# Kernel optimization log

Hardware: AMD Instinct MI355X
Metric: run time of the kernel (lower is better)

Reference implementation:

```python
import jax, jax.numpy as jnp
import numpy as np

B, N, D = 2, 2048, 1024
H, ENC = 16, 8
HD = D // H
EPS = 1e-5


def _apply_rope(x, cos, sin):
    # x: [B,N,H,HD], cos/sin: [N,HD//2]
    c = cos[None, :, None, :]
    s = sin[None, :, None, :]
    x_re = x[..., 0::2]
    x_im = x[..., 1::2]
    out = jnp.stack([x_re * c - x_im * s, x_re * s + x_im * c], axis=-1)
    return out.reshape(x.shape)


def _rmsnorm(x):
    return x * jax.lax.rsqrt(jnp.mean(x * x, axis=-1, keepdims=True) + EPS)


def setup_inputs() -> dict:
    key = jax.random.key(0)
    ks = jax.random.split(key, 8)
    pos = jnp.arange(N, dtype=jnp.float32)[:, None]
    inv_freq = 1.0 / (10000.0 ** (jnp.arange(0, HD, 2, dtype=jnp.float32) / HD))  # [HD//2]
    ang = pos * inv_freq[None, :]
    std = 0.02
    return {
        "x": jax.random.normal(ks[0], (B, N, D), dtype=jnp.float32),
        "rope_cos": jnp.cos(ang),
        "rope_sin": jnp.sin(ang),
        "Wq": std * jax.random.normal(ks[1], (D, D), dtype=jnp.float32),
        "Wk": std * jax.random.normal(ks[2], (D, D), dtype=jnp.float32),
        "Wv": std * jax.random.normal(ks[3], (D, D), dtype=jnp.float32),
        "Wo_enc": std * jax.random.normal(ks[4], (H * HD, D), dtype=jnp.float32),
        "Wo_dec": std * jax.random.normal(ks[5], ((H - ENC) * HD, D), dtype=jnp.float32),
        "heads": H,
        "encoder_heads": ENC,
    }


def reference(x, rope_cos, rope_sin, Wq, Wk, Wv, Wo_enc, Wo_dec, heads, encoder_heads):
    b, n, d = x.shape
    hd = d // heads
    scale = hd ** (-0.5)
    q = (x @ Wq).reshape(b, n, heads, hd)
    k = (x @ Wk).reshape(b, n, heads, hd)
    v = (x @ Wv).reshape(b, n, heads, hd)
    q = _rmsnorm(_apply_rope(q, rope_cos, rope_sin))
    k = _rmsnorm(_apply_rope(k, rope_cos, rope_sin))
    # scores: [B,H,N,N]
    scores = jnp.einsum("bihd,bjhd->bhij", q, k) * scale
    causal = jnp.tril(jnp.ones((n, n), dtype=bool))  # [N,N]
    is_enc = (jnp.arange(heads) < encoder_heads)[:, None, None]  # [H,1,1]
    allow = jnp.logical_or(is_enc, causal[None, :, :])  # [H,N,N]
    scores = jnp.where(allow[None], scores, -jnp.inf)
    att = jax.nn.softmax(scores, axis=-1)
    out = jnp.einsum("bhij,bjhd->bihd", att, v)  # [B,N,H,HD]
    enc_out = out.reshape(b, n, heads * hd) @ Wo_enc
    dec_out = out[:, :, encoder_heads:, :].reshape(b, n, (heads - encoder_heads) * hd) @ Wo_dec
    return (enc_out, dec_out)
```

## Files before the change

kernel.cpp:

```cpp
#include <hip/hip_runtime.h>
#include <hip/hip_bf16.h>
#include <math.h>

#define B_    2
#define N_    2048
#define D_    1024
#define H_    16
#define ENC_  8
#define HD_   64
#define EPS_  1e-5f
#define M_    (B_ * N_)

typedef __bf16 bf16x8 __attribute__((ext_vector_type(8)));
typedef __bf16 bf16x2 __attribute__((ext_vector_type(2)));
typedef float  f32x4  __attribute__((ext_vector_type(4)));

#define MB(x) ((size_t)(x) * 1024 * 1024)

#define KSC_  0.18033688011112042f

__device__ __forceinline__ void gld16(const __bf16* g, __bf16* l) {
    __builtin_amdgcn_global_load_lds(
        (const __attribute__((address_space(1))) void*)g,
        (__attribute__((address_space(3))) void*)l,
        16, 0, 0);
}

template <typename OutT>
__device__ __forceinline__ void gemm_core(
    const __bf16* __restrict__ A, const __bf16* __restrict__ Bt,
    OutT* __restrict__ C, int K, int lda, int aoff, int ldc,
    int bm, int bn, __bf16* As, __bf16* Bs)
{
    const int tid  = threadIdx.x;
    const int w    = tid >> 6;
    const int lane = tid & 63;
    const int lrow = lane & 15;
    const int quad = lane >> 4;
    const int wr   = w >> 1;
    const int wc   = w & 1;

    const int sr = lane >> 2;
    const int sc = (lane & 3) * 8;
    const __bf16* Ag0 = A  + (size_t)(bm +      w * 16 + sr) * lda + aoff + sc;
    const __bf16* Ag1 = A  + (size_t)(bm + 64 + w * 16 + sr) * lda + aoff + sc;
    const __bf16* Bg0 = Bt + (size_t)(bn +      w * 16 + sr) * K + sc;
    const __bf16* Bg1 = Bt + (size_t)(bn + 64 + w * 16 + sr) * K + sc;
    __bf16* Al0 = &As[w * 512];
    __bf16* Al1 = &As[2048 + w * 512];
    __bf16* Bl0 = &Bs[w * 512];
    __bf16* Bl1 = &Bs[2048 + w * 512];

    f32x4 acc[4][4];
    #pragma unroll
    for (int i = 0; i < 4; ++i)
        #pragma unroll
        for (int j = 0; j < 4; ++j) acc[i][j] = (f32x4){0.f, 0.f, 0.f, 0.f};

    for (int k0 = 0; k0 < K; k0 += 32) {
        gld16(Ag0 + k0, Al0);
        gld16(Ag1 + k0, Al1);
        gld16(Bg0 + k0, Bl0);
        gld16(Bg1 + k0, Bl1);
        __syncthreads();

        bf16x8 af[4], bf[4];
        #pragma unroll
        for (int rt = 0; rt < 4; ++rt)
            af[rt] = *(const bf16x8*)&As[(wr * 64 + rt * 16 + lrow) * 32 + quad * 8];
        #pragma unroll
        for (int ct = 0; ct < 4; ++ct)
            bf[ct] = *(const bf16x8*)&Bs[(wc * 64 + ct * 16 + lrow) * 32 + quad * 8];

        #pragma unroll
        for (int rt = 0; rt < 4; ++rt)
            #pragma unroll
            for (int ct = 0; ct < 4; ++ct)
                acc[rt][ct] = __builtin_amdgcn_mfma_f32_16x16x32_bf16(
                    af[rt], bf[ct], acc[rt][ct], 0, 0, 0);
        __syncthreads();
    }

    #pragma unroll
    for (int rt = 0; rt < 4; ++rt)
        #pragma unroll
        for (int ct = 0; ct < 4; ++ct)
            #pragma unroll
            for (int r = 0; r < 4; ++r) {
                const int row = bm + wr * 64 + rt * 16 + quad * 4 + r;
                const int col = bn + wc * 64 + ct * 16 + lrow;
                C[(size_t)row * ldc + col] = (OutT)acc[rt][ct][r];
            }
}

__global__ __launch_bounds__(256) void gemm_qkv(
    const __bf16* __restrict__ A, const __bf16* __restrict__ Bt,
    __bf16* __restrict__ C)
{
    __shared__ __bf16 As[128 * 32];
    __shared__ __bf16 Bs[128 * 32];
    gemm_core<__bf16>(A, Bt, C, D_, D_, 0, 3072,
                      blockIdx.y * 128, blockIdx.x * 128, As, Bs);
}

__global__ __launch_bounds__(256) void gemm_out(
    const __bf16* __restrict__ A, const __bf16* __restrict__ Woe,
    const __bf16* __restrict__ Wod, float* __restrict__ Cenc,
    float* __restrict__ Cdec)
{
    __shared__ __bf16 As[128 * 32];
    __shared__ __bf16 Bs[128 * 32];
    const int bx = blockIdx.x;
    if (bx < 8) {
        gemm_core<float>(A, Woe, Cenc, 1024, D_, 0, D_,
                         blockIdx.y * 128, bx * 128, As, Bs);
    } else {
        gemm_core<float>(A, Wod, Cdec, 512, D_, 512, D_,
                         blockIdx.y * 128, (bx - 8) * 128, As, Bs);
    }
}

__global__ __launch_bounds__(256) void f32_to_bf16(
    const float* __restrict__ src, __bf16* __restrict__ dst)
{
    const size_t i = ((size_t)blockIdx.x * 256 + threadIdx.x) * 8;
    float4 a = *(const float4*)&src[i];
    float4 b = *(const float4*)&src[i + 4];
    bf16x8 o = {(__bf16)a.x, (__bf16)a.y, (__bf16)a.z, (__bf16)a.w,
                (__bf16)b.x, (__bf16)b.y, (__bf16)b.z, (__bf16)b.w};
    *(bf16x8*)&dst[i] = o;
}

struct WtArgs {
    const float* W[5];
    __bf16*      Wt[5];
    int          K[5];
    int          nyb[5];
};

__global__ __launch_bounds__(256) void wt_conv_all(WtArgs a)
{
    const int z = blockIdx.z;
    if (blockIdx.y >= a.nyb[z]) return;
    const float* W  = a.W[z];
    __bf16*      Wt = a.Wt[z];
    const int    K  = a.K[z];

    __shared__ __bf16 t[64][72];
    const int kb = blockIdx.y * 64;
    const int nb = blockIdx.x * 64;
    {
        const int kl = threadIdx.x >> 2;
        const int c0 = (threadIdx.x & 3) * 16;
        const float* src = W + (size_t)(kb + kl) * D_ + nb + c0;
        #pragma unroll
        for (int u = 0; u < 4; ++u) {
            float4 f = *(const float4*)&src[u * 4];
            t[c0 + u * 4 + 0][kl] = (__bf16)f.x;
            t[c0 + u * 4 + 1][kl] = (__bf16)f.y;
            t[c0 + u * 4 + 2][kl] = (__bf16)f.z;
            t[c0 + u * 4 + 3][kl] = (__bf16)f.w;
        }
    }
    __syncthreads();
    {
        const int nl  = threadIdx.x >> 2;
        const int k0c = (threadIdx.x & 3) * 16;
        __bf16* dst = Wt + (size_t)(nb + nl) * K + kb + k0c;
        *(bf16x8*)&dst[0] = *(const bf16x8*)&t[nl][k0c];
        *(bf16x8*)&dst[8] = *(const bf16x8*)&t[nl][k0c + 8];
    }
}

__global__ __launch_bounds__(256) void rope_vconv(
    const __bf16* __restrict__ qkv,
    const float* __restrict__ cs, const float* __restrict__ sn,
    __bf16* __restrict__ qbf, __bf16* __restrict__ kbf,
    __bf16* __restrict__ vt)
{
    if (blockIdx.x < 16384) {
        const int row  = blockIdx.x * 4 + (threadIdx.x >> 6);
        const int lane = threadIdx.x & 63;
        const int n    = (row >> 4) & (N_ - 1);
        const int b    = row >> 15;
        const int h    = row & 15;
        const int p    = lane >> 1;

        const float c = cs[n * (HD_ / 2) + p];
        const float s = sn[n * (HD_ / 2) + p];
        const size_t ibase = (size_t)(b * N_ + n) * 3072 + h * HD_ + lane;
        const size_t obase = ((size_t)(b * H_ + h) * N_ + n) * HD_ + lane;
        const bool odd = (lane & 1);

        {
            float val = (float)qkv[ibase];
            float partner = __shfl_xor(val, 1, 64);
            float r = odd ? fmaf(partner, s, val * c)
                          : (val * c - partner * s);
            float ss = r * r;
            #pragma unroll
            for (int off = 1; off < 64; off <<= 1) ss += __shfl_xor(ss, off, 64);
            qbf[obase] = (__bf16)(r * rsqrtf(ss * (1.0f / 64.0f) + EPS_) * KSC_);
        }
        {
            float val = (float)qkv[ibase + 1024];
            float partner = __shfl_xor(val, 1, 64);
            float r = odd ? fmaf(partner, s, val * c)
                          : (val * c - partner * s);
            float ss = r * r;
            #pragma unroll
            for (int off = 1; off < 64; off <<= 1) ss += __shfl_xor(ss, off, 64);
            kbf[obase] = (__bf16)(r * rsqrtf(ss * (1.0f / 64.0f) + EPS_));
        }
    } else {
        __shared__ __bf16 tile[64][72];
        const int bx = blockIdx.x - 16384;
        const int bh = bx >> 5;
        const int b  = bh >> 4, h = bh & 15;
        const int n0 = (bx & 31) * 64;
        {
            const int nl = threadIdx.x >> 2;
            const int d0 = (threadIdx.x & 3) * 16;
            const __bf16* src =
                qkv + (size_t)(b * N_ + n0 + nl) * 3072 + 2048 + h * HD_ + d0;
            bf16x8 v0 = *(const bf16x8*)&src[0];
            bf16x8 v1 = *(const bf16x8*)&src[8];
            #pragma unroll
            for (int e = 0; e < 8; ++e) {
                tile[d0 + e][nl]     = v0[e];
                tile[d0 + 8 + e][nl] = v1[e];
            }
        }
        __syncthreads();
        {
            const int dl = threadIdx.x >> 2;
            const int nc = (threadIdx.x & 3) * 16;
            __bf16* dst = vt + ((size_t)(bh * HD_ + dl)) * N_ + n0 + nc;
            bf16x8 o0, o1;
            #pragma unroll
            for (int e = 0; e < 8; ++e) {
                const int p0 = nc + e;
                const int p1 = nc + 8 + e;
                o0[e] = tile[dl][(p0 & ~31) + ((p0 & 31) >> 1) + 16 * (p0 & 1)];
                o1[e] = tile[dl][(p1 & ~31) + ((p1 & 31) >> 1) + 16 * (p1 & 1)];
            }
            *(bf16x8*)&dst[0] = o0;
            *(bf16x8*)&dst[8] = o1;
        }
    }
}

__global__ __launch_bounds__(256) void attn_mfma(
    const __bf16* __restrict__ qbf, const __bf16* __restrict__ kbf,
    const __bf16* __restrict__ vtbf, __bf16* __restrict__ o)
{
    __shared__ __bf16 Ks[2][4096];
    __shared__ __bf16 Vs[2][4096];
    __shared__ __bf16 Plds[4][16][36];

    const int tid  = threadIdx.x;
    const int w    = tid >> 6;
    const int lane = tid & 63;
    const int lrow = lane & 15;
    const int quad = lane >> 4;

    int bh, nwork, qbs[2];
    if (blockIdx.x < 512) {
        const int e = blockIdx.x & 15;
        bh = (e >> 3) * 16 + (e & 7);
        qbs[0] = blockIdx.x >> 4;
        qbs[1] = 0;
        nwork = 1;
    } else {
        const int idx = blockIdx.x - 512;
        const int d = idx & 15;
        bh = (d >> 3) * 16 + 8 + (d & 7);
        const int p = idx >> 4;
        qbs[0] = 31 - p;
        qbs[1] = p;
        nwork = 2;
    }
    const int b = bh >> 4, h = bh & 15;
    const bool enc = (h < ENC_);
    const bool dec = !enc;

    const __bf16* qbase = qbf  + (size_t)bh * N_ * HD_;
    const __bf16* kbase = kbf  + (size_t)bh * N_ * HD_;
    const __bf16* vbase = vtbf + (size_t)bh * HD_ * N_;

    const __bf16* kg0 = kbase + (size_t)lane * HD_ + w * 8;
    const __bf16* kg1 = kbase + (size_t)lane * HD_ + (w + 4) * 8;
    const __bf16* vg  = vbase + (size_t)lane * N_;

    const f32x4 zero = {0.f, 0.f, 0.f, 0.f};

    for (int wi = 0; wi < nwork; ++wi) {
        const int qb = qbs[wi];
        const int i0 = qb * 64 + w * 16;
        const int ntiles = enc ? (N_ >> 6) : (qb + 1);

        bf16x8 qf[2];
        #pragma unroll
        for (int kc = 0; kc < 2; ++kc)
            qf[kc] = *(const bf16x8*)
                &qbase[(size_t)(i0 + lrow) * HD_ + kc * 32 + quad * 8];

        f32x4 oacc[4];
        #pragma unroll
        for (int c = 0; c < 4; ++c) oacc[c] = zero;
        float lsum[4] = {};

        auto stage = [&](int t, int bb) {
            const int j0 = t << 6;
            gld16(kg0 + (size_t)j0 * HD_, &Ks[bb][(w)     * 512]);
            gld16(kg1 + (size_t)j0 * HD_, &Ks[bb][(w + 4) * 512]);
            gld16(vg + j0 + w * 8,        &Vs[bb][(w)     * 512]);
            gld16(vg + j0 + (w + 4) * 8,  &Vs[bb][(w + 4) * 512]);
        };

        if (wi) __syncthreads();
        stage(0, 0);
        for (int t = 0; t < ntiles; ++t) {
            const int bb = t & 1;
            __syncthreads();
            if (t + 1 < ntiles) stage(t + 1, bb ^ 1);

            #pragma unroll
            for (int s = 0; s < 2; ++s) {
                const int jp = (t << 6) + s * 32;

                bf16x8 kf0 = *(const bf16x8*)&Ks[bb][((quad)     * 64 + s * 32 + lrow) * 8];
                bf16x8 kf1 = *(const bf16x8*)&Ks[bb][((4 + quad) * 64 + s * 32 + lrow) * 8];
                bf16x8 kf2 = *(const bf16x8*)&Ks[bb][((quad)     * 64 + s * 32 + 16 + lrow) * 8];
                bf16x8 kf3 = *(const bf16x8*)&Ks[bb][((4 + quad) * 64 + s * 32 + 16 + lrow) * 8];

                f32x4 s0 = zero, s1 = zero;
                s0 = __builtin_amdgcn_mfma_f32_16x16x32_bf16(qf[0], kf0, s0, 0, 0, 0);
                s0 = __builtin_amdgcn_mfma_f32_16x16x32_bf16(qf[1], kf1, s0, 0, 0, 0);
                s1 = __builtin_amdgcn_mfma_f32_16x16x32_bf16(qf[0], kf2, s1, 0, 0, 0);
                s1 = __builtin_amdgcn_mfma_f32_16x16x32_bf16(qf[1], kf3, s1, 0, 0, 0);

                if (dec && (jp + 31 > i0)) {
                    #pragma unroll
                    for (int r = 0; r < 4; ++r) {
                        const int i  = i0 + quad * 4 + r;
                        float pA = (jp + lrow      <= i) ? exp2f(s0[r]) : 0.f;
                        float pB = (jp + 16 + lrow <= i) ? exp2f(s1[r]) : 0.f;
                        lsum[r] += pA + pB;
                        bf16x2 pp = {(__bf16)pA, (__bf16)pB};
                        *(bf16x2*)&Plds[w][quad * 4 + r][2 * lrow] = pp;
                    }
                } else {
                    #pragma unroll
                    for (int r = 0; r < 4; ++r) {
                        float pA = exp2f(s0[r]);
                        float pB = exp2f(s1[r]);
                        lsum[r] += pA + pB;
                        bf16x2 pp = {(__bf16)pA, (__bf16)pB};
                        *(bf16x2*)&Plds[w][quad * 4 + r][2 * lrow] = pp;
                    }
                }

                bf16x8 vf0 = *(const bf16x8*)&Vs[bb][((s * 4 + quad) * 64 +  0 + lrow) * 8];
                bf16x8 vf1 = *(const bf16x8*)&Vs[bb][((s * 4 + quad) * 64 + 16 + lrow) * 8];
                bf16x8 vf2 = *(const bf16x8*)&Vs[bb][((s * 4 + quad) * 64 + 32 + lrow) * 8];
                bf16x8 vf3 = *(const bf16x8*)&Vs[bb][((s * 4 + quad) * 64 + 48 + lrow) * 8];

                bf16x8 pf = *(const bf16x8*)&Plds[w][lrow][quad * 8];
                oacc[0] = __builtin_amdgcn_mfma_f32_16x16x32_bf16(pf, vf0, oacc[0], 0, 0, 0);
                oacc[1] = __builtin_amdgcn_mfma_f32_16x16x32_bf16(pf, vf1, oacc[1], 0, 0, 0);
                oacc[2] = __builtin_amdgcn_mfma_f32_16x16x32_bf16(pf, vf2, oacc[2], 0, 0, 0);
                oacc[3] = __builtin_amdgcn_mfma_f32_16x16x32_bf16(pf, vf3, oacc[3], 0, 0, 0);
            }
        }

        #pragma unroll
        for (int r = 0; r < 4; ++r) {
            float s = lsum[r];
            s += __shfl_xor(s, 1, 64);
            s += __shfl_xor(s, 2, 64);
            s += __shfl_xor(s, 4, 64);
            s += __shfl_xor(s, 8, 64);
            lsum[r] = 1.0f / s;
        }

        #pragma unroll
        for (int c = 0; c < 4; ++c)
            #pragma unroll
            for (int r = 0; r < 4; ++r) {
                const int i = i0 + quad * 4 + r;
                o[(size_t)(b * N_ + i) * D_ + h * HD_ + c * 16 + lrow] =
                    (__bf16)(oacc[c][r] * lsum[r]);
            }
    }
}

extern "C" void kernel_launch(void* const* d_in, const int* in_sizes, int n_in,
                              void* d_out, int out_size, void* d_ws, size_t ws_size,
                              hipStream_t stream)
{
    const float* x   = (const float*)d_in[0];
    const float* cs  = (const float*)d_in[1];
    const float* sn  = (const float*)d_in[2];
    const float* Wq  = (const float*)d_in[3];
    const float* Wk  = (const float*)d_in[4];
    const float* Wv  = (const float*)d_in[5];
    const float* Woe = (const float*)d_in[6];
    const float* Wod = (const float*)d_in[7];

    float* enc_out = (float*)d_out;
    float* dec_out = enc_out + (size_t)M_ * D_;

    char* ws = (char*)d_ws;
    __bf16* xbf    = (__bf16*)(ws);
    __bf16* wqkv_t = (__bf16*)(ws + MB(8));
    __bf16* woe_t  = (__bf16*)(ws + MB(14));
    __bf16* wod_t  = (__bf16*)(ws + MB(16));
    __bf16* qkv    = (__bf16*)(ws + MB(17));
    __bf16* qbf    = (__bf16*)(ws + MB(41));
    __bf16* kbf    = (__bf16*)(ws + MB(49));
    __bf16* vtbf   = xbf;
    __bf16* obuf   = qkv;

    f32_to_bf16<<<(M_ * D_) / (256 * 8), 256, 0, stream>>>(x, xbf);

    WtArgs wa;
    wa.W[0] = Wq;  wa.Wt[0] = wqkv_t;                 wa.K[0] = 1024; wa.nyb[0] = 16;
    wa.W[1] = Wk;  wa.Wt[1] = wqkv_t + 1024 * 1024;   wa.K[1] = 1024; wa.nyb[1] = 16;
    wa.W[2] = Wv;  wa.Wt[2] = wqkv_t + 2048 * 1024;   wa.K[2] = 1024; wa.nyb[2] = 16;
    wa.W[3] = Woe; wa.Wt[3] = woe_t;                  wa.K[3] = 1024; wa.nyb[3] = 16;
    wa.W[4] = Wod; wa.Wt[4] = wod_t;                  wa.K[4] = 512;  wa.nyb[4] = 8;
    wt_conv_all<<<dim3(16, 16, 5), 256, 0, stream>>>(wa);

    gemm_qkv<<<dim3(3072 / 128, M_ / 128), 256, 0, stream>>>(xbf, wqkv_t, qkv);

    rope_vconv<<<16384 + 1024, 256, 0, stream>>>(qkv, cs, sn, qbf, kbf, vtbf);

    attn_mfma<<<dim3(768), 256, 0, stream>>>(qbf, kbf, vtbf, obuf);

    gemm_out<<<dim3(16, M_ / 128), 256, 0, stream>>>(
        obuf, woe_t, wod_t, enc_out, dec_out);
}
```

Measured before the change: 236.4 us.

## Load K fragments directly to registers and give each decoder query block its own workgroup

```diff
diff --git a/kernel.cpp b/kernel.cpp
--- a/kernel.cpp
+++ b/kernel.cpp
@@ -18,6 +18,12 @@
 #define MB(x) ((size_t)(x) * 1024 * 1024)
 
 #define KSC_  0.18033688011112042f
+
+#if __has_builtin(__builtin_amdgcn_exp2f)
+#define EXP2F(x) __builtin_amdgcn_exp2f(x)
+#else
+#define EXP2F(x) exp2f(x)
+#endif
 
 __device__ __forceinline__ void gld16(const __bf16* g, __bf16* l) {
     __builtin_amdgcn_global_load_lds(
@@ -254,7 +260,6 @@
     const __bf16* __restrict__ qbf, const __bf16* __restrict__ kbf,
     const __bf16* __restrict__ vtbf, __bf16* __restrict__ o)
 {
-    __shared__ __bf16 Ks[2][4096];
     __shared__ __bf16 Vs[2][4096];
     __shared__ __bf16 Plds[4][16][36];
 
@@ -264,21 +269,16 @@
     const int lrow = lane & 15;
     const int quad = lane >> 4;
 
-    int bh, nwork, qbs[2];
+    int bh, qb;
     if (blockIdx.x < 512) {
         const int e = blockIdx.x & 15;
         bh = (e >> 3) * 16 + (e & 7);
-        qbs[0] = blockIdx.x >> 4;
-        qbs[1] = 0;
-        nwork = 1;
+        qb = blockIdx.x >> 4;
     } else {
         const int idx = blockIdx.x - 512;
         const int d = idx & 15;
         bh = (d >> 3) * 16 + 8 + (d & 7);
-        const int p = idx >> 4;
-        qbs[0] = 31 - p;
-        qbs[1] = p;
-        nwork = 2;
+        qb = 31 - (idx >> 4);
     }
     const int b = bh >> 4, h = bh & 15;
     const bool enc = (h < ENC_);
@@ -288,111 +288,112 @@
     const __bf16* kbase = kbf  + (size_t)bh * N_ * HD_;
     const __bf16* vbase = vtbf + (size_t)bh * HD_ * N_;
 
-    const __bf16* kg0 = kbase + (size_t)lane * HD_ + w * 8;
-    const __bf16* kg1 = kbase + (size_t)lane * HD_ + (w + 4) * 8;
-    const __bf16* vg  = vbase + (size_t)lane * N_;
+    const __bf16* vg = vbase + (size_t)lane * N_;
+
+    const int i0 = qb * 64 + w * 16;
+    const int ntiles = enc ? (N_ >> 6) : (qb + 1);
+
+    bf16x8 qf[2];
+    #pragma unroll
+    for (int kc = 0; kc < 2; ++kc)
+        qf[kc] = *(const bf16x8*)
+            &qbase[(size_t)(i0 + lrow) * HD_ + kc * 32 + quad * 8];
 
     const f32x4 zero = {0.f, 0.f, 0.f, 0.f};
-
-    for (int wi = 0; wi < nwork; ++wi) {
-        const int qb = qbs[wi];
-        const int i0 = qb * 64 + w * 16;
-        const int ntiles = enc ? (N_ >> 6) : (qb + 1);
-
-        bf16x8 qf[2];
-        #pragma unroll
-        for (int kc = 0; kc < 2; ++kc)
-            qf[kc] = *(const bf16x8*)
-                &qbase[(size_t)(i0 + lrow) * HD_ + kc * 32 + quad * 8];
-
-        f32x4 oacc[4];
-        #pragma unroll
-        for (int c = 0; c < 4; ++c) oacc[c] = zero;
-        float lsum[4] = {};
-
-        auto stage = [&](int t, int bb) {
-            const int j0 = t << 6;
-            gld16(kg0 + (size_t)j0 * HD_, &Ks[bb][(w)     * 512]);
-            gld16(kg1 + (size_t)j0 * HD_, &Ks[bb][(w + 4) * 512]);
-            gld16(vg + j0 + w * 8,        &Vs[bb][(w)     * 512]);
-            gld16(vg + j0 + (w + 4) * 8,  &Vs[bb][(w + 4) * 512]);
-        };
-
-        if (wi) __syncthreads();
-        stage(0, 0);
-        for (int t = 0; t < ntiles; ++t) {
-            const int bb = t & 1;
-            __syncthreads();
-            if (t + 1 < ntiles) stage(t + 1, bb ^ 1);
-
-            #pragma unroll
-            for (int s = 0; s < 2; ++s) {
-                const int jp = (t << 6) + s * 32;
-
-                bf16x8 kf0 = *(const bf16x8*)&Ks[bb][((quad)     * 64 + s * 32 + lrow) * 8];
-                bf16x8 kf1 = *(const bf16x8*)&Ks[bb][((4 + quad) * 64 + s * 32 + lrow) * 8];
-                bf16x8 kf2 = *(const bf16x8*)&Ks[bb][((quad)     * 64 + s * 32 + 16 + lrow) * 8];
-                bf16x8 kf3 = *(const bf16x8*)&Ks[bb][((4 + quad) * 64 + s * 32 + 16 + lrow) * 8];
-
-                f32x4 s0 = zero, s1 = zero;
-                s0 = __builtin_amdgcn_mfma_f32_16x16x32_bf16(qf[0], kf0, s0, 0, 0, 0);
-                s0 = __builtin_amdgcn_mfma_f32_16x16x32_bf16(qf[1], kf1, s0, 0, 0, 0);
-                s1 = __builtin_amdgcn_mfma_f32_16x16x32_bf16(qf[0], kf2, s1, 0, 0, 0);
-                s1 = __builtin_amdgcn_mfma_f32_16x16x32_bf16(qf[1], kf3, s1, 0, 0, 0);
-
-                if (dec && (jp + 31 > i0)) {
-                    #pragma unroll
-                    for (int r = 0; r < 4; ++r) {
-                        const int i  = i0 + quad * 4 + r;
-                        float pA = (jp + lrow      <= i) ? exp2f(s0[r]) : 0.f;
-                        float pB = (jp + 16 + lrow <= i) ? exp2f(s1[r]) : 0.f;
-                        lsum[r] += pA + pB;
-                        bf16x2 pp = {(__bf16)pA, (__bf16)pB};
-                        *(bf16x2*)&Plds[w][quad * 4 + r][2 * lrow] = pp;
-                    }
-                } else {
-                    #pragma unroll
-                    for (int r = 0; r < 4; ++r) {
-                        float pA = exp2f(s0[r]);
-                        float pB = exp2f(s1[r]);
-                        lsum[r] += pA + pB;
-                        bf16x2 pp = {(__bf16)pA, (__bf16)pB};
-                        *(bf16x2*)&Plds[w][quad * 4 + r][2 * lrow] = pp;
-                    }
+    f32x4 oacc[4];
+    #pragma unroll
+    for (int c = 0; c < 4; ++c) oacc[c] = zero;
+    float lsum[4] = {};
+
+    bf16x8 kf[8];
+    const __bf16* kfb = kbase + (size_t)lrow * HD_ + quad * 8;
+    auto loadKhalf = [&](int t, int half) {
+        const __bf16* kp = kfb + (size_t)((t << 6) + half * 32) * HD_;
+        kf[half * 4 + 0] = *(const bf16x8*)(kp);
+        kf[half * 4 + 1] = *(const bf16x8*)(kp + 32);
+        kf[half * 4 + 2] = *(const bf16x8*)(kp + 16 * HD_);
+        kf[half * 4 + 3] = *(const bf16x8*)(kp + 16 * HD_ + 32);
+    };
+
+    auto stageV = [&](int t, int bb) {
+        const int j0 = t << 6;
+        gld16(vg + j0 + w * 8,       &Vs[bb][(w)     * 512]);
+        gld16(vg + j0 + (w + 4) * 8, &Vs[bb][(w + 4) * 512]);
+    };
+
+    loadKhalf(0, 0);
+    loadKhalf(0, 1);
+    stageV(0, 0);
+    for (int t = 0; t < ntiles; ++t) {
+        const int bb = t & 1;
+        __syncthreads();
+        if (t + 1 < ntiles) stageV(t + 1, bb ^ 1);
+        const int tn = (t + 1 < ntiles) ? t + 1 : t;
+
+        #pragma unroll
+        for (int s = 0; s < 2; ++s) {
+            const int jp = (t << 6) + s * 32;
+
+            f32x4 s0 = zero, s1 = zero;
+            s0 = __builtin_amdgcn_mfma_f32_16x16x32_bf16(qf[0], kf[s*4+0], s0, 0, 0, 0);
+            s0 = __builtin_amdgcn_mfma_f32_16x16x32_bf16(qf[1], kf[s*4+1], s0, 0, 0, 0);
+            s1 = __builtin_amdgcn_mfma_f32_16x16x32_bf16(qf[0], kf[s*4+2], s1, 0, 0, 0);
+            s1 = __builtin_amdgcn_mfma_f32_16x16x32_bf16(qf[1], kf[s*4+3], s1, 0, 0, 0);
+
+            loadKhalf(tn, s);
+
+            if (dec && (jp + 31 > i0)) {
+                #pragma unroll
+                for (int r = 0; r < 4; ++r) {
+                    const int i  = i0 + quad * 4 + r;
+                    float pA = (jp + lrow      <= i) ? EXP2F(s0[r]) : 0.f;
+                    float pB = (jp + 16 + lrow <= i) ? EXP2F(s1[r]) : 0.f;
+                    lsum[r] += pA + pB;
+                    bf16x2 pp = {(__bf16)pA, (__bf16)pB};
+                    *(bf16x2*)&Plds[w][quad * 4 + r][2 * lrow] = pp;
                 }
-
-                bf16x8 vf0 = *(const bf16x8*)&Vs[bb][((s * 4 + quad) * 64 +  0 + lrow) * 8];
-                bf16x8 vf1 = *(const bf16x8*)&Vs[bb][((s * 4 + quad) * 64 + 16 + lrow) * 8];
-                bf16x8 vf2 = *(const bf16x8*)&Vs[bb][((s * 4 + quad) * 64 + 32 + lrow) * 8];
-                bf16x8 vf3 = *(const bf16x8*)&Vs[bb][((s * 4 + quad) * 64 + 48 + lrow) * 8];
-
-                bf16x8 pf = *(const bf16x8*)&Plds[w][lrow][quad * 8];
-                oacc[0] = __builtin_amdgcn_mfma_f32_16x16x32_bf16(pf, vf0, oacc[0], 0, 0, 0);
-                oacc[1] = __builtin_amdgcn_mfma_f32_16x16x32_bf16(pf, vf1, oacc[1], 0, 0, 0);
-                oacc[2] = __builtin_amdgcn_mfma_f32_16x16x32_bf16(pf, vf2, oacc[2], 0, 0, 0);
-                oacc[3] = __builtin_amdgcn_mfma_f32_16x16x32_bf16(pf, vf3, oacc[3], 0, 0, 0);
+            } else {
+                #pragma unroll
+                for (int r = 0; r < 4; ++r) {
+                    float pA = EXP2F(s0[r]);
+                    float pB = EXP2F(s1[r]);
+                    lsum[r] += pA + pB;
+                    bf16x2 pp = {(__bf16)pA, (__bf16)pB};
+                    *(bf16x2*)&Plds[w][quad * 4 + r][2 * lrow] = pp;
+                }
             }
-        }
-
+
+            bf16x8 vf0 = *(const bf16x8*)&Vs[bb][((s * 4 + quad) * 64 +  0 + lrow) * 8];
+            bf16x8 vf1 = *(const bf16x8*)&Vs[bb][((s * 4 + quad) * 64 + 16 + lrow) * 8];
+            bf16x8 vf2 = *(const bf16x8*)&Vs[bb][((s * 4 + quad) * 64 + 32 + lrow) * 8];
+            bf16x8 vf3 = *(const bf16x8*)&Vs[bb][((s * 4 + quad) * 64 + 48 + lrow) * 8];
+
+            bf16x8 pf = *(const bf16x8*)&Plds[w][lrow][quad * 8];
+            oacc[0] = __builtin_amdgcn_mfma_f32_16x16x32_bf16(pf, vf0, oacc[0], 0, 0, 0);
+            oacc[1] = __builtin_amdgcn_mfma_f32_16x16x32_bf16(pf, vf1, oacc[1], 0, 0, 0);
+            oacc[2] = __builtin_amdgcn_mfma_f32_16x16x32_bf16(pf, vf2, oacc[2], 0, 0, 0);
+            oacc[3] = __builtin_amdgcn_mfma_f32_16x16x32_bf16(pf, vf3, oacc[3], 0, 0, 0);
+        }
+    }
+
+    #pragma unroll
+    for (int r = 0; r < 4; ++r) {
+        float s = lsum[r];
+        s += __shfl_xor(s, 1, 64);
+        s += __shfl_xor(s, 2, 64);
+        s += __shfl_xor(s, 4, 64);
+        s += __shfl_xor(s, 8, 64);
+        lsum[r] = 1.0f / s;
+    }
+
+    #pragma unroll
+    for (int c = 0; c < 4; ++c)
         #pragma unroll
         for (int r = 0; r < 4; ++r) {
-            float s = lsum[r];
-            s += __shfl_xor(s, 1, 64);
-            s += __shfl_xor(s, 2, 64);
-            s += __shfl_xor(s, 4, 64);
-            s += __shfl_xor(s, 8, 64);
-            lsum[r] = 1.0f / s;
-        }
-
-        #pragma unroll
-        for (int c = 0; c < 4; ++c)
-            #pragma unroll
-            for (int r = 0; r < 4; ++r) {
-                const int i = i0 + quad * 4 + r;
-                o[(size_t)(b * N_ + i) * D_ + h * HD_ + c * 16 + lrow] =
-                    (__bf16)(oacc[c][r] * lsum[r]);
-            }
-    }
+            const int i = i0 + quad * 4 + r;
+            o[(size_t)(b * N_ + i) * D_ + h * HD_ + c * 16 + lrow] =
+                (__bf16)(oacc[c][r] * lsum[r]);
+        }
 }
 
 extern "C" void kernel_launch(void* const* d_in, const int* in_sizes, int n_in,
@@ -436,7 +437,7 @@
 
     rope_vconv<<<16384 + 1024, 256, 0, stream>>>(qkv, cs, sn, qbf, kbf, vtbf);
 
-    attn_mfma<<<dim3(768), 256, 0, stream>>>(qbf, kbf, vtbf, obuf);
+    attn_mfma<<<dim3(1024), 256, 0, stream>>>(qbf, kbf, vtbf, obuf);
 
     gemm_out<<<dim3(16, M_ / 128), 256, 0, stream>>>(
         obuf, woe_t, wod_t, enc_out, dec_out);
```

Result: slower. 310.5 us (+31.4%).

## Process two query tiles per encoder block and split decoder pairing

Applied to the files above, without the earlier changes.

```diff
diff --git a/kernel.cpp b/kernel.cpp
--- a/kernel.cpp
+++ b/kernel.cpp
@@ -18,6 +18,12 @@
 #define MB(x) ((size_t)(x) * 1024 * 1024)
 
 #define KSC_  0.18033688011112042f
+
+#if __has_builtin(__builtin_amdgcn_exp2f)
+#define EXP2F(x) __builtin_amdgcn_exp2f(x)
+#else
+#define EXP2F(x) exp2f(x)
+#endif
 
 __device__ __forceinline__ void gld16(const __bf16* g, __bf16* l) {
     __builtin_amdgcn_global_load_lds(
@@ -250,148 +256,175 @@
     }
 }
 
-__global__ __launch_bounds__(256) void attn_mfma(
-    const __bf16* __restrict__ qbf, const __bf16* __restrict__ kbf,
-    const __bf16* __restrict__ vtbf, __bf16* __restrict__ o)
-{
-    __shared__ __bf16 Ks[2][4096];
-    __shared__ __bf16 Vs[2][4096];
-    __shared__ __bf16 Plds[4][16][36];
-
+template <int NG, bool DEC>
+__device__ __forceinline__ void attn_core(
+    const __bf16* __restrict__ qbase, const __bf16* __restrict__ kbase,
+    const __bf16* __restrict__ vbase, __bf16* __restrict__ o,
+    int b, int h, int qb, int ntiles,
+    __bf16 (*Ks)[4096], __bf16 (*Vs)[4096], __bf16* P)
+{
     const int tid  = threadIdx.x;
     const int w    = tid >> 6;
     const int lane = tid & 63;
     const int lrow = lane & 15;
     const int quad = lane >> 4;
 
-    int bh, nwork, qbs[2];
-    if (blockIdx.x < 512) {
-        const int e = blockIdx.x & 15;
-        bh = (e >> 3) * 16 + (e & 7);
-        qbs[0] = blockIdx.x >> 4;
-        qbs[1] = 0;
-        nwork = 1;
-    } else {
-        const int idx = blockIdx.x - 512;
-        const int d = idx & 15;
-        bh = (d >> 3) * 16 + 8 + (d & 7);
-        const int p = idx >> 4;
-        qbs[0] = 31 - p;
-        qbs[1] = p;
-        nwork = 2;
-    }
-    const int b = bh >> 4, h = bh & 15;
-    const bool enc = (h < ENC_);
-    const bool dec = !enc;
-
-    const __bf16* qbase = qbf  + (size_t)bh * N_ * HD_;
-    const __bf16* kbase = kbf  + (size_t)bh * N_ * HD_;
-    const __bf16* vbase = vtbf + (size_t)bh * HD_ * N_;
-
     const __bf16* kg0 = kbase + (size_t)lane * HD_ + w * 8;
     const __bf16* kg1 = kbase + (size_t)lane * HD_ + (w + 4) * 8;
     const __bf16* vg  = vbase + (size_t)lane * N_;
 
+    int i0g[NG];
+    #pragma unroll
+    for (int g = 0; g < NG; ++g) i0g[g] = qb * (NG * 64) + g * 64 + w * 16;
+
+    bf16x8 qf[NG][2];
+    #pragma unroll
+    for (int g = 0; g < NG; ++g)
+        #pragma unroll
+        for (int kc = 0; kc < 2; ++kc)
+            qf[g][kc] = *(const bf16x8*)
+                &qbase[(size_t)(i0g[g] + lrow) * HD_ + kc * 32 + quad * 8];
+
     const f32x4 zero = {0.f, 0.f, 0.f, 0.f};
-
-    for (int wi = 0; wi < nwork; ++wi) {
-        const int qb = qbs[wi];
-        const int i0 = qb * 64 + w * 16;
-        const int ntiles = enc ? (N_ >> 6) : (qb + 1);
-
-        bf16x8 qf[2];
-        #pragma unroll
-        for (int kc = 0; kc < 2; ++kc)
-            qf[kc] = *(const bf16x8*)
-                &qbase[(size_t)(i0 + lrow) * HD_ + kc * 32 + quad * 8];
-
-        f32x4 oacc[4];
-        #pragma unroll
-        for (int c = 0; c < 4; ++c) oacc[c] = zero;
-        float lsum[4] = {};
-
-        auto stage = [&](int t, int bb) {
-            const int j0 = t << 6;
-            gld16(kg0 + (size_t)j0 * HD_, &Ks[bb][(w)     * 512]);
-            gld16(kg1 + (size_t)j0 * HD_, &Ks[bb][(w + 4) * 512]);
-            gld16(vg + j0 + w * 8,        &Vs[bb][(w)     * 512]);
-            gld16(vg + j0 + (w + 4) * 8,  &Vs[bb][(w + 4) * 512]);
-        };
-
-        if (wi) __syncthreads();
-        stage(0, 0);
-        for (int t = 0; t < ntiles; ++t) {
-            const int bb = t & 1;
-            __syncthreads();
-            if (t + 1 < ntiles) stage(t + 1, bb ^ 1);
-
-            #pragma unroll
-            for (int s = 0; s < 2; ++s) {
-                const int jp = (t << 6) + s * 32;
-
-                bf16x8 kf0 = *(const bf16x8*)&Ks[bb][((quad)     * 64 + s * 32 + lrow) * 8];
-                bf16x8 kf1 = *(const bf16x8*)&Ks[bb][((4 + quad) * 64 + s * 32 + lrow) * 8];
-                bf16x8 kf2 = *(const bf16x8*)&Ks[bb][((quad)     * 64 + s * 32 + 16 + lrow) * 8];
-                bf16x8 kf3 = *(const bf16x8*)&Ks[bb][((4 + quad) * 64 + s * 32 + 16 + lrow) * 8];
-
-                f32x4 s0 = zero, s1 = zero;
-                s0 = __builtin_amdgcn_mfma_f32_16x16x32_bf16(qf[0], kf0, s0, 0, 0, 0);
-                s0 = __builtin_amdgcn_mfma_f32_16x16x32_bf16(qf[1], kf1, s0, 0, 0, 0);
-                s1 = __builtin_amdgcn_mfma_f32_16x16x32_bf16(qf[0], kf2, s1, 0, 0, 0);
-                s1 = __builtin_amdgcn_mfma_f32_16x16x32_bf16(qf[1], kf3, s1, 0, 0, 0);
-
-                if (dec && (jp + 31 > i0)) {
+    f32x4 oacc[NG][4];
+    float lsum[NG][4];
+    #pragma unroll
+    for (int g = 0; g < NG; ++g)
+        #pragma unroll
+        for (int c = 0; c < 4; ++c) { oacc[g][c] = zero; lsum[g][c] = 0.f; }
+
+    auto stage = [&](int t, int bb) {
+        const int j0 = t << 6;
+        gld16(kg0 + (size_t)j0 * HD_, &Ks[bb][(w)     * 512]);
+        gld16(kg1 + (size_t)j0 * HD_, &Ks[bb][(w + 4) * 512]);
+        gld16(vg + j0 + w * 8,        &Vs[bb][(w)     * 512]);
+        gld16(vg + j0 + (w + 4) * 8,  &Vs[bb][(w + 4) * 512]);
+    };
+
+    stage(0, 0);
+    for (int t = 0; t < ntiles; ++t) {
+        const int bb = t & 1;
+        __syncthreads();
+        if (t + 1 < ntiles) stage(t + 1, bb ^ 1);
+
+        #pragma unroll
+        for (int s = 0; s < 2; ++s) {
+            const int jp = (t << 6) + s * 32;
+
+            bf16x8 kf0 = *(const bf16x8*)&Ks[bb][((quad)     * 64 + s * 32 + lrow) * 8];
+            bf16x8 kf1 = *(const bf16x8*)&Ks[bb][((4 + quad) * 64 + s * 32 + lrow) * 8];
+            bf16x8 kf2 = *(const bf16x8*)&Ks[bb][((quad)     * 64 + s * 32 + 16 + lrow) * 8];
+            bf16x8 kf3 = *(const bf16x8*)&Ks[bb][((4 + quad) * 64 + s * 32 + 16 + lrow) * 8];
+
+            f32x4 s0[NG], s1[NG];
+            #pragma unroll
+            for (int g = 0; g < NG; ++g) { s0[g] = zero; s1[g] = zero; }
+            #pragma unroll
+            for (int g = 0; g < NG; ++g)
+                s0[g] = __builtin_amdgcn_mfma_f32_16x16x32_bf16(qf[g][0], kf0, s0[g], 0, 0, 0);
+            #pragma unroll
+            for (int g = 0; g < NG; ++g)
+                s0[g] = __builtin_amdgcn_mfma_f32_16x16x32_bf16(qf[g][1], kf1, s0[g], 0, 0, 0);
+            #pragma unroll
+            for (int g = 0; g < NG; ++g)
+                s1[g] = __builtin_amdgcn_mfma_f32_16x16x32_bf16(qf[g][0], kf2, s1[g], 0, 0, 0);
+            #pragma unroll
+            for (int g = 0; g < NG; ++g)
+                s1[g] = __builtin_amdgcn_mfma_f32_16x16x32_bf16(qf[g][1], kf3, s1[g], 0, 0, 0);
+
+            #pragma unroll
+            for (int g = 0; g < NG; ++g) {
+                __bf16* Pg = P + ((w * NG + g) * 16) * 36;
+                if (DEC && (jp + 31 > i0g[g])) {
                     #pragma unroll
                     for (int r = 0; r < 4; ++r) {
-                        const int i  = i0 + quad * 4 + r;
-                        float pA = (jp + lrow      <= i) ? exp2f(s0[r]) : 0.f;
-                        float pB = (jp + 16 + lrow <= i) ? exp2f(s1[r]) : 0.f;
-                        lsum[r] += pA + pB;
+                        const int i  = i0g[g] + quad * 4 + r;
+                        float pA = (jp + lrow      <= i) ? EXP2F(s0[g][r]) : 0.f;
+                        float pB = (jp + 16 + lrow <= i) ? EXP2F(s1[g][r]) : 0.f;
+                        lsum[g][r] += pA + pB;
                         bf16x2 pp = {(__bf16)pA, (__bf16)pB};
-                        *(bf16x2*)&Plds[w][quad * 4 + r][2 * lrow] = pp;
+                        *(bf16x2*)&Pg[(quad * 4 + r) * 36 + 2 * lrow] = pp;
                     }
                 } else {
                     #pragma unroll
                     for (int r = 0; r < 4; ++r) {
-                        float pA = exp2f(s0[r]);
-                        float pB = exp2f(s1[r]);
-                        lsum[r] += pA + pB;
+                        float pA = EXP2F(s0[g][r]);
+                        float pB = EXP2F(s1[g][r]);
+                        lsum[g][r] += pA + pB;
                         bf16x2 pp = {(__bf16)pA, (__bf16)pB};
-                        *(bf16x2*)&Plds[w][quad * 4 + r][2 * lrow] = pp;
+                        *(bf16x2*)&Pg[(quad * 4 + r) * 36 + 2 * lrow] = pp;
                     }
                 }
-
-                bf16x8 vf0 = *(const bf16x8*)&Vs[bb][((s * 4 + quad) * 64 +  0 + lrow) * 8];
-                bf16x8 vf1 = *(const bf16x8*)&Vs[bb][((s * 4 + quad) * 64 + 16 + lrow) * 8];
-                bf16x8 vf2 = *(const bf16x8*)&Vs[bb][((s * 4 + quad) * 64 + 32 + lrow) * 8];
-                bf16x8 vf3 = *(const bf16x8*)&Vs[bb][((s * 4 + quad) * 64 + 48 + lrow) * 8];
-
-                bf16x8 pf = *(const bf16x8*)&Plds[w][lrow][quad * 8];
-                oacc[0] = __builtin_amdgcn_mfma_f32_16x16x32_bf16(pf, vf0, oacc[0], 0, 0, 0);
-                oacc[1] = __builtin_amdgcn_mfma_f32_16x16x32_bf16(pf, vf1, oacc[1], 0, 0, 0);
-                oacc[2] = __builtin_amdgcn_mfma_f32_16x16x32_bf16(pf, vf2, oacc[2], 0, 0, 0);
-                oacc[3] = __builtin_amdgcn_mfma_f32_16x16x32_bf16(pf, vf3, oacc[3], 0, 0, 0);
-            }
-        }
-
+            }
+
+            bf16x8 vf0 = *(const bf16x8*)&Vs[bb][((s * 4 + quad) * 64 +  0 + lrow) * 8];
+            bf16x8 vf1 = *(const bf16x8*)&Vs[bb][((s * 4 + quad) * 64 + 16 + lrow) * 8];
+            bf16x8 vf2 = *(const bf16x8*)&Vs[bb][((s * 4 + quad) * 64 + 32 + lrow) * 8];
+            bf16x8 vf3 = *(const bf16x8*)&Vs[bb][((s * 4 + quad) * 64 + 48 + lrow) * 8];
+
+            bf16x8 pf[NG];
+            #pragma unroll
+            for (int g = 0; g < NG; ++g)
+                pf[g] = *(const bf16x8*)&P[((w * NG + g) * 16 + lrow) * 36 + quad * 8];
+            #pragma unroll
+            for (int g = 0; g < NG; ++g) {
+                oacc[g][0] = __builtin_amdgcn_mfma_f32_16x16x32_bf16(pf[g], vf0, oacc[g][0], 0, 0, 0);
+                oacc[g][1] = __builtin_amdgcn_mfma_f32_16x16x32_bf16(pf[g], vf1, oacc[g][1], 0, 0, 0);
+                oacc[g][2] = __builtin_amdgcn_mfma_f32_16x16x32_bf16(pf[g], vf2, oacc[g][2], 0, 0, 0);
+                oacc[g][3] = __builtin_amdgcn_mfma_f32_16x16x32_bf16(pf[g], vf3, oacc[g][3], 0, 0, 0);
+            }
+        }
+    }
+
+    #pragma unroll
+    for (int g = 0; g < NG; ++g)
         #pragma unroll
         for (int r = 0; r < 4; ++r) {
-            float s = lsum[r];
+            float s = lsum[g][r];
             s += __shfl_xor(s, 1, 64);
             s += __shfl_xor(s, 2, 64);
             s += __shfl_xor(s, 4, 64);
             s += __shfl_xor(s, 8, 64);
-            lsum[r] = 1.0f / s;
-        }
-
+            lsum[g][r] = 1.0f / s;
+        }
+
+    #pragma unroll
+    for (int g = 0; g < NG; ++g)
         #pragma unroll
         for (int c = 0; c < 4; ++c)
             #pragma unroll
             for (int r = 0; r < 4; ++r) {
-                const int i = i0 + quad * 4 + r;
+                const int i = i0g[g] + quad * 4 + r;
                 o[(size_t)(b * N_ + i) * D_ + h * HD_ + c * 16 + lrow] =
-                    (__bf16)(oacc[c][r] * lsum[r]);
-            }
+                    (__bf16)(oacc[g][c][r] * lsum[g][r]);
+            }
+}
+
+__global__ __launch_bounds__(256) void attn_mfma(
+    const __bf16* __restrict__ qbf, const __bf16* __restrict__ kbf,
+    const __bf16* __restrict__ vtbf, __bf16* __restrict__ o)
+{
+    __shared__ __bf16 Ks[2][4096];
+    __shared__ __bf16 Vs[2][4096];
+    __shared__ __bf16 P[4 * 2 * 16 * 36];
+
+    if (blockIdx.x < 256) {
+        const int e  = blockIdx.x & 15;
+        const int bh = (e >> 3) * 16 + (e & 7);
+        const int qb = blockIdx.x >> 4;
+        attn_core<2, false>(
+            qbf  + (size_t)bh * N_ * HD_, kbf + (size_t)bh * N_ * HD_,
+            vtbf + (size_t)bh * HD_ * N_, o,
+            bh >> 4, bh & 15, qb, N_ >> 6, Ks, Vs, P);
+    } else {
+        const int idx = blockIdx.x - 256;
+        const int d   = idx & 15;
+        const int bh  = (d >> 3) * 16 + 8 + (d & 7);
+        const int qb  = 31 - (idx >> 4);
+        attn_core<1, true>(
+            qbf  + (size_t)bh * N_ * HD_, kbf + (size_t)bh * N_ * HD_,
+            vtbf + (size_t)bh * HD_ * N_, o,
+            bh >> 4, bh & 15, qb, qb + 1, Ks, Vs, P);
     }
 }
 
```

New measurement: 237.2 us. About the same (+0.4%).
